# Performance work log

Measured on AMD Instinct MI355X. Metric: run time of the kernel, lower is better.

Reference implementation:

```python
import jax, jax.numpy as jnp
import numpy as np

N_NODES = 50000
N_EDGES = 800000
N_GRAPHS = 512
D_NODE = 64
D_EDGE = 32
Z_DIM = 2 * D_NODE + D_EDGE  # 160


def setup_inputs() -> dict:
    key = jax.random.key(0)
    ks = jax.random.split(key, 12)
    inp = {
        'x': jax.random.normal(ks[0], (N_NODES, D_NODE), dtype=jnp.float32),
        'edge_index': jax.random.randint(ks[1], (2, N_EDGES), 0, N_NODES, dtype=jnp.int64),
        'edge_attr': jax.random.uniform(ks[2], (N_EDGES, D_EDGE), dtype=jnp.float32),
        'batch': jnp.sort(jax.random.randint(ks[3], (N_NODES,), 0, N_GRAPHS, dtype=jnp.int64)),
        'Wf1': jax.random.normal(ks[4], (Z_DIM, D_NODE), dtype=jnp.float32) * 0.05,
        'bf1': jnp.zeros((D_NODE,), dtype=jnp.float32),
        'Ws1': jax.random.normal(ks[5], (Z_DIM, D_NODE), dtype=jnp.float32) * 0.05,
        'bs1': jnp.zeros((D_NODE,), dtype=jnp.float32),
        'Wf2': jax.random.normal(ks[6], (Z_DIM, D_NODE), dtype=jnp.float32) * 0.05,
        'bf2': jnp.zeros((D_NODE,), dtype=jnp.float32),
        'Ws2': jax.random.normal(ks[7], (Z_DIM, D_NODE), dtype=jnp.float32) * 0.05,
        'bs2': jnp.zeros((D_NODE,), dtype=jnp.float32),
        'W_out': jax.random.normal(ks[8], (D_NODE, 1), dtype=jnp.float32) * 0.05,
        'b_out': jnp.zeros((1,), dtype=jnp.float32),
    }
    return inp


def _cgconv(x, edge_index, edge_attr, Wf, bf, Ws, bs):
    # PyG CGConv: out_i = x_i + sum_{j in N(i)} sigmoid(lin_f(z_ij)) * softplus(lin_s(z_ij))
    # with z_ij = [x_i, x_j, e_ij]; source_to_target flow: j=edge_index[0], i=edge_index[1]
    src, dst = edge_index[0], edge_index[1]
    z = jnp.concatenate([x[dst], x[src], edge_attr], axis=-1)  # [E, 2d+dim]
    msg = jax.nn.sigmoid(z @ Wf + bf) * jax.nn.softplus(z @ Ws + bs)  # [E, d]
    aggr = jax.ops.segment_sum(msg, dst, num_segments=x.shape[0])
    return x + aggr


def reference(x, edge_index, edge_attr, batch, Wf1, bf1, Ws1, bs1, Wf2, bf2, Ws2, bs2, W_out, b_out):
    h = _cgconv(x, edge_index, edge_attr, Wf1, bf1, Ws1, bs1)
    h = _cgconv(h, edge_index, edge_attr, Wf2, bf2, Ws2, bs2)
    pooled = jax.ops.segment_sum(h, batch, num_segments=N_GRAPHS)  # global_add_pool [G, d]
    out = pooled @ W_out + b_out  # [G, 1]
    return out
```

## Files before the change

### kernel.cpp

```cpp
#include <hip/hip_runtime.h>
#include <math.h>

#define N_NODES 50000
#define N_EDGES 800000
#define N_GRAPHS 512
#define D 64
#define DE 32
#define NTILE (N_EDGES / 16)
#define NB_SCAN 196
#define LSTR 68
#define NSTR 136


typedef __attribute__((ext_vector_type(8))) short short8;
typedef __attribute__((ext_vector_type(4))) float floatx4;
union Frag { short8 s; unsigned u[4]; };
union U4   { uint4 v; unsigned u[4]; };

__device__ inline unsigned pk_bf16(float lo, float hi) {
    unsigned a = __float_as_uint(lo);
    unsigned b = __float_as_uint(hi);
    a = (a + 0x7FFFu + ((a >> 16) & 1u)) >> 16;
    b = (b + 0x7FFFu + ((b >> 16) & 1u)) >> 16;
    return a | (b << 16);
}
__device__ inline unsigned short bf16_1(float v) {
    unsigned a = __float_as_uint(v);
    return (unsigned short)((a + 0x7FFFu + ((a >> 16) & 1u)) >> 16);
}
__device__ inline float upk(unsigned u16) { return __uint_as_float(u16 << 16); }

__global__ __launch_bounds__(256) void hist_kernel(
    const int* __restrict__ ei, int* __restrict__ deg)
{
    int e = blockIdx.x * 256 + threadIdx.x;
    atomicAdd(&deg[ei[N_EDGES + e]], 1);
}

__global__ __launch_bounds__(256) void scan1(
    const int* __restrict__ deg, int* __restrict__ off, int* __restrict__ tsum)
{
    __shared__ int s[256];
    int i = blockIdx.x * 256 + threadIdx.x;
    s[threadIdx.x] = (i < N_NODES) ? deg[i] : 0;
    __syncthreads();
    if (threadIdx.x == 0) {
        int run = 0;
        for (int k = 0; k < 256; ++k) { int t = s[k]; s[k] = run; run += t; }
        tsum[blockIdx.x] = run;
    }
    __syncthreads();
    if (i < N_NODES) off[i] = s[threadIdx.x];
}

__global__ __launch_bounds__(256) void scan2(int* __restrict__ tsum)
{
    __shared__ int s[256];
    int i = threadIdx.x;
    s[i] = (i < NB_SCAN) ? tsum[i] : 0;
    __syncthreads();
    if (i == 0) {
        int run = 0;
        for (int k = 0; k < NB_SCAN; ++k) { int t = s[k]; s[k] = run; run += t; }
    }
    __syncthreads();
    if (i < NB_SCAN) tsum[i] = s[i];
}

__global__ __launch_bounds__(256) void scan3(
    int* __restrict__ off, const int* __restrict__ tsum)
{
    int i = blockIdx.x * 256 + threadIdx.x;
    if (i < N_NODES) off[i] += tsum[blockIdx.x];
    if (i == N_NODES) off[i] = N_EDGES;
}

__global__ __launch_bounds__(256) void scatter_pack(
    const int* __restrict__ ei, const int* __restrict__ off,
    int* __restrict__ cnt, const float* __restrict__ ea,
    unsigned short* __restrict__ eaS,
    int2* __restrict__ sd_sorted)
{
    int e = blockIdx.x * 256 + threadIdx.x;
    int s = ei[e];
    int d = ei[N_EDGES + e];
    int r = atomicAdd(&cnt[d], 1);
    int pos = off[d] + r;
    sd_sorted[pos] = make_int2(s, d);

    const float4* src4 = (const float4*)(ea + (size_t)e * 32);
    uint4* dst16 = (uint4*)(eaS + (size_t)pos * 32);
#pragma unroll
    for (int q = 0; q < 2; ++q) {
        float4 v0 = src4[4 * q + 0];
        float4 v1 = src4[4 * q + 1];
        float4 v2 = src4[4 * q + 2];
        float4 v3 = src4[4 * q + 3];
        uint4 o0;
        o0.x = pk_bf16(v0.x, v0.y); o0.y = pk_bf16(v0.z, v0.w);
        o0.z = pk_bf16(v1.x, v1.y); o0.w = pk_bf16(v1.z, v1.w);
        uint4 o1;
        o1.x = pk_bf16(v2.x, v2.y); o1.y = pk_bf16(v2.z, v2.w);
        o1.z = pk_bf16(v3.x, v3.y); o1.w = pk_bf16(v3.z, v3.w);
        dst16[2 * q + 0] = o0;
        dst16[2 * q + 1] = o1;
    }
}

__global__ __launch_bounds__(256) void node_transform_mfma(
    const float* __restrict__ H,
    const float* __restrict__ Wf,
    const float* __restrict__ Ws,
    const float* __restrict__ bf,
    const float* __restrict__ bs,
    unsigned short* __restrict__ Tdst,
    unsigned short* __restrict__ Tsrc,
    float* __restrict__ hinit)
{
    __shared__ unsigned short lt[4][16 * NSTR];
    const int lane = threadIdx.x & 63;
    const int wid  = threadIdx.x >> 6;
    const int n16  = lane & 15;
    const int quad = lane >> 4;
    const int kc   = quad * 8;
    unsigned short* L = lt[wid];

    const int gid = blockIdx.x * 4 + wid;
    const int NW  = (N_NODES / 16) * 2;
    if (gid >= NW) return;
    const int ntile = gid >> 1;
    const int part  = gid & 1;
    unsigned short* Tout = part ? Tsrc : Tdst;
    const int rbase = part * 64;

    const float* hrow = H + (size_t)(ntile * 16 + n16) * D;
    float4 q0 = *(const float4*)(hrow + kc);
    float4 q1 = *(const float4*)(hrow + kc + 4);
    float4 q2 = *(const float4*)(hrow + 32 + kc);
    float4 q3 = *(const float4*)(hrow + 32 + kc + 4);
    Frag a0, a1;
    a0.u[0] = pk_bf16(q0.x, q0.y); a0.u[1] = pk_bf16(q0.z, q0.w);
    a0.u[2] = pk_bf16(q1.x, q1.y); a0.u[3] = pk_bf16(q1.z, q1.w);
    a1.u[0] = pk_bf16(q2.x, q2.y); a1.u[1] = pk_bf16(q2.z, q2.w);
    a1.u[2] = pk_bf16(q3.x, q3.y); a1.u[3] = pk_bf16(q3.z, q3.w);

    if (part == 0) {
        float4* hp = (float4*)(hinit + (size_t)(ntile * 16 + n16) * D);
        hp[quad * 2]     = q0;
        hp[quad * 2 + 1] = q1;
        hp[8 + quad * 2] = q2;
        hp[9 + quad * 2] = q3;
    }

#pragma unroll
    for (int cbi = 0; cbi < 8; ++cbi) {
        const int col   = cbi * 16 + n16;
        const int sflag = col & 1;
        const int j     = col >> 1;
        const float* Wsel = sflag ? Ws : Wf;

        Frag b0, b1;
        {
            float t0[8], t1[8];
#pragma unroll
            for (int i = 0; i < 8; ++i) {
                t0[i] = Wsel[(rbase + kc + i) * 64 + j];
                t1[i] = Wsel[(rbase + 32 + kc + i) * 64 + j];
            }
#pragma unroll
            for (int p = 0; p < 4; ++p) {
                b0.u[p] = pk_bf16(t0[2 * p], t0[2 * p + 1]);
                b1.u[p] = pk_bf16(t1[2 * p], t1[2 * p + 1]);
            }
        }
        float bias = 0.0f;
        if (part == 0) bias = sflag ? bs[j] : bf[j];

        floatx4 acc = {bias, bias, bias, bias};
        acc = __builtin_amdgcn_mfma_f32_16x16x32_bf16(a0.s, b0.s, acc, 0, 0, 0);
        acc = __builtin_amdgcn_mfma_f32_16x16x32_bf16(a1.s, b1.s, acc, 0, 0, 0);

#pragma unroll
        for (int r = 0; r < 4; ++r)
            L[(quad * 4 + r) * NSTR + col] = bf16_1(acc[r]);
    }

#pragma unroll
    for (int it = 0; it < 4; ++it) {
        const int node_l = it * 4 + quad;
        const int c8     = n16 * 8;
        uint4 v = *(const uint4*)(L + node_l * NSTR + c8);
        *(uint4*)(Tout + (size_t)(ntile * 16 + node_l) * 128 + c8) = v;
    }
}

__global__ __launch_bounds__(256) void edge_message_mfma(
    const unsigned short* __restrict__ Tdst,
    const unsigned short* __restrict__ Tsrc,
    const unsigned short* __restrict__ eaS,
    const int2* __restrict__ sd_sorted,
    const float* __restrict__ Wf,
    const float* __restrict__ Ws,
    float* __restrict__ hout)
{
    __shared__ float lds[4][16 * LSTR];
    const int lane = threadIdx.x & 63;
    const int wid  = threadIdx.x >> 6;
    const int n16  = lane & 15;
    const int quad = lane >> 4;
    const int c0   = quad * 8;
    float* L = lds[wid];

    Frag bfr[4], bsr[4];
#pragma unroll
    for (int jb = 0; jb < 4; ++jb) {
        const int j = n16 * 4 + jb;
        float tf[8], tsv[8];
#pragma unroll
        for (int i = 0; i < 8; ++i) {
            tf[i]  = Wf[(128 + c0 + i) * 64 + j];
            tsv[i] = Ws[(128 + c0 + i) * 64 + j];
        }
#pragma unroll
        for (int p = 0; p < 4; ++p) {
            bfr[jb].u[p] = pk_bf16(tf[2 * p], tf[2 * p + 1]);
            bsr[jb].u[p] = pk_bf16(tsv[2 * p], tsv[2 * p + 1]);
        }
    }

    const floatx4 zero = {0.0f, 0.0f, 0.0f, 0.0f};
    const int nwaves = gridDim.x * 4;
    for (int t = blockIdx.x * 4 + wid; t < NTILE; t += nwaves) {
        const int p0 = t * 16;

        const int2 sd = sd_sorted[p0 + n16];
        const int sv16 = sd.x;
        const int dv16 = sd.y;

        Frag af;
        af.s = *(const short8*)(eaS + (size_t)(p0 + n16) * 32 + c0);

        floatx4 accf[4], accs[4];
#pragma unroll
        for (int jb = 0; jb < 4; ++jb) {
            accf[jb] = __builtin_amdgcn_mfma_f32_16x16x32_bf16(af.s, bfr[jb].s, zero, 0, 0, 0);
            accs[jb] = __builtin_amdgcn_mfma_f32_16x16x32_bf16(af.s, bsr[jb].s, zero, 0, 0, 0);
        }

        U4 s4[4], d4[4];
#pragma unroll
        for (int r = 0; r < 4; ++r) {
            const int m = quad * 4 + r;
            const int sv = __shfl(sv16, m);
            const int dv = __shfl(dv16, m);
            s4[r].v = *(const uint4*)(Tsrc + (size_t)sv * 128 + n16 * 8);
            d4[r].v = *(const uint4*)(Tdst + (size_t)dv * 128 + n16 * 8);
        }

#pragma unroll
        for (int r = 0; r < 4; ++r) {
            const int m = quad * 4 + r;
            float4 msg;
            float* mp = (float*)&msg;
#pragma unroll
            for (int jb = 0; jb < 4; ++jb) {
                unsigned d2 = d4[r].u[jb];
                unsigned s2 = s4[r].u[jb];
                float vf = accf[jb][r] + upk(d2 & 0xFFFFu) + upk(s2 & 0xFFFFu);
                float vs = accs[jb][r] + upk(d2 >> 16) + upk(s2 >> 16);
                float sig = __builtin_amdgcn_rcpf(1.0f + __expf(-vf));
                float spl = fmaxf(vs, 0.0f) + __logf(1.0f + __expf(-fabsf(vs)));
                mp[jb] = sig * spl;
            }
            *(float4*)(L + m * LSTR + n16 * 4) = msg;
        }

        {
            int cur = __builtin_amdgcn_readlane(dv16, 0);
            float acc = L[0 * LSTR + lane];
#pragma unroll
            for (int r = 1; r < 16; ++r) {
                int d = __builtin_amdgcn_readlane(dv16, r);
                float v = L[r * LSTR + lane];
                if (d != cur) {
                    atomicAdd(&hout[(size_t)cur * D + lane], acc);
                    cur = d; acc = v;
                } else {
                    acc += v;
                }
            }
            atomicAdd(&hout[(size_t)cur * D + lane], acc);
        }
    }
}

__global__ __launch_bounds__(256) void pool_kernel(
    const float* __restrict__ h,
    const int* __restrict__ batch,
    float* __restrict__ pooled)
{
    const int lane = threadIdx.x & 63;
    const int wid  = threadIdx.x >> 6;
    const int w = blockIdx.x * 4 + wid;
    const int n0 = w * 16;
    if (n0 >= N_NODES) return;
    const int nend = (n0 + 16 < N_NODES) ? (n0 + 16) : N_NODES;

    int cur = batch[n0];
    float acc = 0.0f;
    for (int n = n0; n < nend; ++n) {
        int b = batch[n];
        float v = h[(size_t)n * D + lane];
        if (b != cur) {
            atomicAdd(&pooled[(size_t)cur * D + lane], acc);
            cur = b; acc = v;
        } else {
            acc += v;
        }
    }
    atomicAdd(&pooled[(size_t)cur * D + lane], acc);
}

__global__ __launch_bounds__(256) void out_kernel(
    const float* __restrict__ pooled,
    const float* __restrict__ Wout,
    const float* __restrict__ bout,
    float* __restrict__ out)
{
    const int g = blockIdx.x * blockDim.x + threadIdx.x;
    if (g >= N_GRAPHS) return;
    float acc = bout[0];
#pragma unroll
    for (int j = 0; j < D; ++j) acc = fmaf(pooled[(size_t)g * D + j], Wout[j], acc);
    out[g] = acc;
}

extern "C" void kernel_launch(void* const* d_in, const int* in_sizes, int n_in,
                              void* d_out, int out_size, void* d_ws, size_t ws_size,
                              hipStream_t stream) {
    const float* x     = (const float*)d_in[0];
    const int*   ei    = (const int*)  d_in[1];
    const float* ea    = (const float*)d_in[2];
    const int*   batch = (const int*)  d_in[3];
    const float* Wf1   = (const float*)d_in[4];
    const float* bf1   = (const float*)d_in[5];
    const float* Ws1   = (const float*)d_in[6];
    const float* bs1   = (const float*)d_in[7];
    const float* Wf2   = (const float*)d_in[8];
    const float* bf2   = (const float*)d_in[9];
    const float* Ws2   = (const float*)d_in[10];
    const float* bs2   = (const float*)d_in[11];
    const float* Wout  = (const float*)d_in[12];
    const float* bout  = (const float*)d_in[13];
    float* out = (float*)d_out;

    char* base = (char*)d_ws;
    size_t o = 0;
    unsigned short* Tdst = (unsigned short*)(base + o); o += (size_t)N_NODES * 128 * 2;
    unsigned short* Tsrc = (unsigned short*)(base + o); o += (size_t)N_NODES * 128 * 2;
    unsigned short* eaS  = (unsigned short*)(base + o); o += (size_t)N_EDGES * 32 * 2;
    float* h1     = (float*)(base + o); o += (size_t)N_NODES * D * 4;
    float* h2     = (float*)(base + o); o += (size_t)N_NODES * D * 4;
    float* pooled = (float*)(base + o); o += (size_t)N_GRAPHS * D * 4;
    int* deg  = (int*)(base + o); o += (size_t)N_NODES * 4;
    int* off  = (int*)(base + o); o += (size_t)(N_NODES + 1) * 4;
    int* tsum = (int*)(base + o); o += 256 * 4;
    int2* sd_sorted = (int2*)(base + o); o += (size_t)N_EDGES * 8;

    hipMemsetAsync(deg, 0, (size_t)N_NODES * 4, stream);
    hist_kernel<<<N_EDGES / 256, 256, 0, stream>>>(ei, deg);
    scan1<<<NB_SCAN, 256, 0, stream>>>(deg, off, tsum);
    scan2<<<1, 256, 0, stream>>>(tsum);
    scan3<<<NB_SCAN, 256, 0, stream>>>(off, tsum);
    hipMemsetAsync(deg, 0, (size_t)N_NODES * 4, stream);
    scatter_pack<<<N_EDGES / 256, 256, 0, stream>>>(ei, off, deg, ea, eaS, sd_sorted);

    node_transform_mfma<<<1563, 256, 0, stream>>>(x, Wf1, Ws1, bf1, bs1, Tdst, Tsrc, h1);
    edge_message_mfma<<<3125, 256, 0, stream>>>(Tdst, Tsrc, eaS,
                                                sd_sorted, Wf1, Ws1, h1);

    node_transform_mfma<<<1563, 256, 0, stream>>>(h1, Wf2, Ws2, bf2, bs2, Tdst, Tsrc, h2);
    edge_message_mfma<<<3125, 256, 0, stream>>>(Tdst, Tsrc, eaS,
                                                sd_sorted, Wf2, Ws2, h2);

    hipMemsetAsync(pooled, 0, (size_t)N_GRAPHS * D * 4, stream);
    pool_kernel<<<782, 256, 0, stream>>>(h2, batch, pooled);
    out_kernel<<<2, 256, 0, stream>>>(pooled, Wout, bout, out);
}
```

Baseline: 505.3 us.

## Prepack bf16 weight fragments and aggregate edge messages in registers with XCD-aware tiles

Adds a pack_W kernel that converts both layers' weights into bf16 MFMA fragment layout once, so the node and edge kernels load ready fragments instead of gathering and converting fp32 weights in every wave. The edge kernel drops the LDS staging and wave-wide segmented reduction. Each lane now keeps running sums for its 4 columns across consecutive dst-sorted edges, reloads the Tdst row only when dst changes, and flushes with atomics. Tiles are assigned contiguously per XCD, with 4 tiles per wave, to improve L2 locality. In exchange it adds 4x more atomics per flush (per quad lane rather than per lane row), serial per-row dependence, and fixed 4-tile coverage that relies on the grid exactly matching NTILE.

```diff
diff --git a/kernel.cpp b/kernel.cpp
--- a/kernel.cpp
+++ b/kernel.cpp
@@ -8,7 +8,6 @@
 #define DE 32
 #define NTILE (N_EDGES / 16)
 #define NB_SCAN 196
-#define LSTR 68
 #define NSTR 136
 
 
@@ -107,12 +106,58 @@
     }
 }
 
+__global__ __launch_bounds__(256) void pack_W(
+    const float* __restrict__ Wf1, const float* __restrict__ Ws1,
+    const float* __restrict__ Wf2, const float* __restrict__ Ws2,
+    uint4* __restrict__ WpkNT, uint4* __restrict__ WpkE)
+{
+    const int layer = blockIdx.y;
+    const float* Wf = layer ? Wf2 : Wf1;
+    const float* Ws = layer ? Ws2 : Ws1;
+    const int i = blockIdx.x * 256 + threadIdx.x;
+    if (i < 1024) {
+        const int p    = i >> 9;
+        const int cbi  = (i >> 6) & 7;
+        const int l    = i & 63;
+        const int n16  = l & 15, quad = l >> 4, kc = quad * 8;
+        const int col  = cbi * 16 + n16;
+        const int j    = col >> 1;
+        const float* Wsel = (col & 1) ? Ws : Wf;
+        const int rbase = p * 64;
+        U4 b0, b1;
+#pragma unroll
+        for (int pp = 0; pp < 4; ++pp) {
+            b0.u[pp] = pk_bf16(Wsel[(rbase + kc + 2 * pp) * 64 + j],
+                               Wsel[(rbase + kc + 2 * pp + 1) * 64 + j]);
+            b1.u[pp] = pk_bf16(Wsel[(rbase + 32 + kc + 2 * pp) * 64 + j],
+                               Wsel[(rbase + 32 + kc + 2 * pp + 1) * 64 + j]);
+        }
+        uint4* o = WpkNT + ((size_t)layer * 1024 + i) * 2;
+        o[0] = b0.v; o[1] = b1.v;
+    } else if (i < 1280) {
+        const int k  = i - 1024;
+        const int jb = k >> 6;
+        const int l  = k & 63;
+        const int n16 = l & 15, quad = l >> 4, c0 = quad * 8;
+        const int j = n16 * 4 + jb;
+        U4 bf_, bs_;
+#pragma unroll
+        for (int pp = 0; pp < 4; ++pp) {
+            bf_.u[pp] = pk_bf16(Wf[(128 + c0 + 2 * pp) * 64 + j],
+                                Wf[(128 + c0 + 2 * pp + 1) * 64 + j]);
+            bs_.u[pp] = pk_bf16(Ws[(128 + c0 + 2 * pp) * 64 + j],
+                                Ws[(128 + c0 + 2 * pp + 1) * 64 + j]);
+        }
+        uint4* o = WpkE + ((size_t)layer * 256 + k) * 2;
+        o[0] = bf_.v; o[1] = bs_.v;
+    }
+}
+
 __global__ __launch_bounds__(256) void node_transform_mfma(
     const float* __restrict__ H,
-    const float* __restrict__ Wf,
-    const float* __restrict__ Ws,
     const float* __restrict__ bf,
     const float* __restrict__ bs,
+    const uint4* __restrict__ Wpk,
     unsigned short* __restrict__ Tdst,
     unsigned short* __restrict__ Tsrc,
     float* __restrict__ hinit)
@@ -131,7 +176,6 @@
     const int ntile = gid >> 1;
     const int part  = gid & 1;
     unsigned short* Tout = part ? Tsrc : Tdst;
-    const int rbase = part * 64;
 
     const float* hrow = H + (size_t)(ntile * 16 + n16) * D;
     float4 q0 = *(const float4*)(hrow + kc);
@@ -157,21 +201,12 @@
         const int col   = cbi * 16 + n16;
         const int sflag = col & 1;
         const int j     = col >> 1;
-        const float* Wsel = sflag ? Ws : Wf;
 
         Frag b0, b1;
         {
-            float t0[8], t1[8];
-#pragma unroll
-            for (int i = 0; i < 8; ++i) {
-                t0[i] = Wsel[(rbase + kc + i) * 64 + j];
-                t1[i] = Wsel[(rbase + 32 + kc + i) * 64 + j];
-            }
-#pragma unroll
-            for (int p = 0; p < 4; ++p) {
-                b0.u[p] = pk_bf16(t0[2 * p], t0[2 * p + 1]);
-                b1.u[p] = pk_bf16(t1[2 * p], t1[2 * p + 1]);
-            }
+            const uint4* bp = Wpk + ((size_t)(part * 512 + cbi * 64 + lane)) * 2;
+            *(uint4*)&b0 = bp[0];
+            *(uint4*)&b1 = bp[1];
         }
         float bias = 0.0f;
         if (part == 0) bias = sflag ? bs[j] : bf[j];
@@ -199,43 +234,38 @@
     const unsigned short* __restrict__ Tsrc,
     const unsigned short* __restrict__ eaS,
     const int2* __restrict__ sd_sorted,
-    const float* __restrict__ Wf,
-    const float* __restrict__ Ws,
+    const uint4* __restrict__ WpkE,
     float* __restrict__ hout)
 {
-    __shared__ float lds[4][16 * LSTR];
     const int lane = threadIdx.x & 63;
     const int wid  = threadIdx.x >> 6;
     const int n16  = lane & 15;
     const int quad = lane >> 4;
     const int c0   = quad * 8;
-    float* L = lds[wid];
 
     Frag bfr[4], bsr[4];
 #pragma unroll
     for (int jb = 0; jb < 4; ++jb) {
-        const int j = n16 * 4 + jb;
-        float tf[8], tsv[8];
-#pragma unroll
-        for (int i = 0; i < 8; ++i) {
-            tf[i]  = Wf[(128 + c0 + i) * 64 + j];
-            tsv[i] = Ws[(128 + c0 + i) * 64 + j];
-        }
-#pragma unroll
-        for (int p = 0; p < 4; ++p) {
-            bfr[jb].u[p] = pk_bf16(tf[2 * p], tf[2 * p + 1]);
-            bsr[jb].u[p] = pk_bf16(tsv[2 * p], tsv[2 * p + 1]);
-        }
-    }
+        *(uint4*)&bfr[jb] = WpkE[((size_t)(jb * 64 + lane)) * 2 + 0];
+        *(uint4*)&bsr[jb] = WpkE[((size_t)(jb * 64 + lane)) * 2 + 1];
+    }
+
+    const int nwg = gridDim.x;
+    const int xcd = blockIdx.x & 7;
+    const int idx = blockIdx.x >> 3;
+    const int q   = nwg >> 3, rr = nwg & 7;
+    const int sb  = (xcd < rr ? xcd * (q + 1) : rr * (q + 1) + (xcd - rr) * q) + idx;
+    const int t0  = (sb * 4 + wid) * 4;
 
     const floatx4 zero = {0.0f, 0.0f, 0.0f, 0.0f};
-    const int nwaves = gridDim.x * 4;
-    for (int t = blockIdx.x * 4 + wid; t < NTILE; t += nwaves) {
-        const int p0 = t * 16;
-
-        const int2 sd = sd_sorted[p0 + n16];
-        const int sv16 = sd.x;
-        const int dv16 = sd.y;
+
+    int   cur_d = -1;
+    U4    dreg; dreg.v = make_uint4(0u, 0u, 0u, 0u);
+    float acc0 = 0.f, acc1 = 0.f, acc2 = 0.f, acc3 = 0.f;
+
+#pragma unroll 1
+    for (int tt = 0; tt < 4; ++tt) {
+        const int p0 = (t0 + tt) * 16;
 
         Frag af;
         af.s = *(const short8*)(eaS + (size_t)(p0 + n16) * 32 + c0);
@@ -247,50 +277,48 @@
             accs[jb] = __builtin_amdgcn_mfma_f32_16x16x32_bf16(af.s, bsr[jb].s, zero, 0, 0, 0);
         }
 
-        U4 s4[4], d4[4];
+        const int2* sdq = sd_sorted + p0 + quad * 4;
+
 #pragma unroll
         for (int r = 0; r < 4; ++r) {
-            const int m = quad * 4 + r;
-            const int sv = __shfl(sv16, m);
-            const int dv = __shfl(dv16, m);
-            s4[r].v = *(const uint4*)(Tsrc + (size_t)sv * 128 + n16 * 8);
-            d4[r].v = *(const uint4*)(Tdst + (size_t)dv * 128 + n16 * 8);
-        }
-
-#pragma unroll
-        for (int r = 0; r < 4; ++r) {
-            const int m = quad * 4 + r;
-            float4 msg;
-            float* mp = (float*)&msg;
+            const int2 sdm = sdq[r];
+            U4 s4;
+            s4.v = *(const uint4*)(Tsrc + (size_t)sdm.x * 128 + n16 * 8);
+            const int dv = sdm.y;
+            if (dv != cur_d) {
+                if (cur_d >= 0) {
+                    float* hp = hout + (size_t)cur_d * D + n16 * 4;
+                    atomicAdd(hp + 0, acc0);
+                    atomicAdd(hp + 1, acc1);
+                    atomicAdd(hp + 2, acc2);
+                    atomicAdd(hp + 3, acc3);
+                }
+                cur_d = dv;
+                dreg.v = *(const uint4*)(Tdst + (size_t)dv * 128 + n16 * 8);
+                acc0 = acc1 = acc2 = acc3 = 0.f;
+            }
 #pragma unroll
             for (int jb = 0; jb < 4; ++jb) {
-                unsigned d2 = d4[r].u[jb];
-                unsigned s2 = s4[r].u[jb];
+                unsigned d2 = dreg.u[jb];
+                unsigned s2 = s4.u[jb];
                 float vf = accf[jb][r] + upk(d2 & 0xFFFFu) + upk(s2 & 0xFFFFu);
                 float vs = accs[jb][r] + upk(d2 >> 16) + upk(s2 >> 16);
                 float sig = __builtin_amdgcn_rcpf(1.0f + __expf(-vf));
                 float spl = fmaxf(vs, 0.0f) + __logf(1.0f + __expf(-fabsf(vs)));
-                mp[jb] = sig * spl;
+                float msg = sig * spl;
+                if      (jb == 0) acc0 += msg;
+                else if (jb == 1) acc1 += msg;
+                else if (jb == 2) acc2 += msg;
+                else              acc3 += msg;
             }
-            *(float4*)(L + m * LSTR + n16 * 4) = msg;
-        }
-
-        {
-            int cur = __builtin_amdgcn_readlane(dv16, 0);
-            float acc = L[0 * LSTR + lane];
-#pragma unroll
-            for (int r = 1; r < 16; ++r) {
-                int d = __builtin_amdgcn_readlane(dv16, r);
-                float v = L[r * LSTR + lane];
-                if (d != cur) {
-                    atomicAdd(&hout[(size_t)cur * D + lane], acc);
-                    cur = d; acc = v;
-                } else {
-                    acc += v;
-                }
-            }
-            atomicAdd(&hout[(size_t)cur * D + lane], acc);
-        }
+        }
+    }
+    {
+        float* hp = hout + (size_t)cur_d * D + n16 * 4;
+        atomicAdd(hp + 0, acc0);
+        atomicAdd(hp + 1, acc1);
+        atomicAdd(hp + 2, acc2);
+        atomicAdd(hp + 3, acc3);
     }
 }
 
@@ -366,6 +394,10 @@
     int* off  = (int*)(base + o); o += (size_t)(N_NODES + 1) * 4;
     int* tsum = (int*)(base + o); o += 256 * 4;
     int2* sd_sorted = (int2*)(base + o); o += (size_t)N_EDGES * 8;
+    uint4* WpkNT = (uint4*)(base + o); o += (size_t)2 * 1024 * 2 * 16;
+    uint4* WpkE  = (uint4*)(base + o); o += (size_t)2 * 256 * 2 * 16;
+
+    pack_W<<<dim3(5, 2), 256, 0, stream>>>(Wf1, Ws1, Wf2, Ws2, WpkNT, WpkE);
 
     hipMemsetAsync(deg, 0, (size_t)N_NODES * 4, stream);
     hist_kernel<<<N_EDGES / 256, 256, 0, stream>>>(ei, deg);
@@ -375,13 +407,13 @@
     hipMemsetAsync(deg, 0, (size_t)N_NODES * 4, stream);
     scatter_pack<<<N_EDGES / 256, 256, 0, stream>>>(ei, off, deg, ea, eaS, sd_sorted);
 
-    node_transform_mfma<<<1563, 256, 0, stream>>>(x, Wf1, Ws1, bf1, bs1, Tdst, Tsrc, h1);
-    edge_message_mfma<<<3125, 256, 0, stream>>>(Tdst, Tsrc, eaS,
-                                                sd_sorted, Wf1, Ws1, h1);
-
-    node_transform_mfma<<<1563, 256, 0, stream>>>(h1, Wf2, Ws2, bf2, bs2, Tdst, Tsrc, h2);
-    edge_message_mfma<<<3125, 256, 0, stream>>>(Tdst, Tsrc, eaS,
-                                                sd_sorted, Wf2, Ws2, h2);
+    node_transform_mfma<<<1563, 256, 0, stream>>>(x, bf1, bs1, WpkNT, Tdst, Tsrc, h1);
+    edge_message_mfma<<<3125, 256, 0, stream>>>(Tdst, Tsrc, eaS, sd_sorted,
+                                                WpkE, h1);
+
+    node_transform_mfma<<<1563, 256, 0, stream>>>(h1, bf2, bs2, WpkNT + 2048, Tdst, Tsrc, h2);
+    edge_message_mfma<<<3125, 256, 0, stream>>>(Tdst, Tsrc, eaS, sd_sorted,
+                                                WpkE + 512, h2);
 
     hipMemsetAsync(pooled, 0, (size_t)N_GRAPHS * D * 4, stream);
     pool_kernel<<<782, 256, 0, stream>>>(h2, batch, pooled);
```

Result: slower. 736.7 us (+45.8%).
